# Optimization experiments

Hardware: AMD Instinct MI355X
Metric: run time of the kernel (lower is better)

Reference implementation:

```python
import jax, jax.numpy as jnp
import numpy as np

T, B, Y = 256, 2048, 20   # time, batch, y_dim
H = 256                   # rnn_macro_dim
HD = 256                  # h_dim (decoder MLP)
N_LAYERS = 2


def _gru_cell(x, h, Wih, Whh, bih, bhh):
    # PyTorch GRU cell. Wih: [3H, in], Whh: [3H, H]; gate order r, z, n.
    gx = x @ Wih.T + bih            # [B, 3H]
    gh = h @ Whh.T + bhh            # [B, 3H]
    gx_r, gx_z, gx_n = jnp.split(gx, 3, axis=-1)
    gh_r, gh_z, gh_n = jnp.split(gh, 3, axis=-1)
    r = jax.nn.sigmoid(gx_r + gh_r)
    z = jax.nn.sigmoid(gx_z + gh_z)
    n = jnp.tanh(gx_n + r * gh_n)
    return (1.0 - z) * n + z * h


def setup_inputs() -> dict:
    key = jax.random.key(0)
    ks = jax.random.split(key, 16)
    s = 0.05
    inp = {
        'data': jax.random.normal(ks[0], (T, B, Y), dtype=jnp.float32),
        # GRU layer 0 (input Y) and layer 1 (input H)
        'Wih0': jax.random.normal(ks[1], (3 * H, Y), dtype=jnp.float32) * s,
        'Whh0': jax.random.normal(ks[2], (3 * H, H), dtype=jnp.float32) * s,
        'bih0': jax.random.normal(ks[3], (3 * H,), dtype=jnp.float32) * s,
        'bhh0': jax.random.normal(ks[4], (3 * H,), dtype=jnp.float32) * s,
        'Wih1': jax.random.normal(ks[5], (3 * H, H), dtype=jnp.float32) * s,
        'Whh1': jax.random.normal(ks[6], (3 * H, H), dtype=jnp.float32) * s,
        'bih1': jax.random.normal(ks[7], (3 * H,), dtype=jnp.float32) * s,
        'bhh1': jax.random.normal(ks[8], (3 * H,), dtype=jnp.float32) * s,
        # dec_macro: Linear(H, HD) -> ReLU -> Linear(HD, HD) -> ReLU -> Linear(HD, Y)
        'W1': jax.random.normal(ks[9], (HD, H), dtype=jnp.float32) * s,
        'b1': jax.random.normal(ks[10], (HD,), dtype=jnp.float32) * s,
        'W2': jax.random.normal(ks[11], (HD, HD), dtype=jnp.float32) * s,
        'b2': jax.random.normal(ks[12], (HD,), dtype=jnp.float32) * s,
        'W3': jax.random.normal(ks[13], (Y, HD), dtype=jnp.float32) * s,
        'b3': jax.random.normal(ks[14], (Y,), dtype=jnp.float32) * s,
    }
    return inp


def reference(data, Wih0, Whh0, bih0, bhh0, Wih1, Whh1, bih1, bhh1,
              W1, b1, W2, b2, W3, b3):
    # hp['train'] == 'macro' branch of PROG_RNN_DET.forward
    batch = data.shape[1]
    h_init = jnp.zeros((N_LAYERS, batch, H), dtype=data.dtype)

    def step(h, xs):
        x_t, next_t = xs
        h0 = _gru_cell(x_t, h[0], Wih0, Whh0, bih0, bhh0)
        h1 = _gru_cell(h0, h[1], Wih1, Whh1, bih1, bhh1)
        d = jax.nn.relu(h1 @ W1.T + b1)
        d = jax.nn.relu(d @ W2.T + b2)
        d = d @ W3.T + b3
        loss_t = jnp.sum((d - next_t) ** 2)
        return jnp.stack([h0, h1]), loss_t

    _, losses = jax.lax.scan(step, h_init, (data[:-1], data[1:]))
    return jnp.sum(losses)
```

## Files before the change

### kernel.cpp

```cpp
#include <hip/hip_runtime.h>
#include <stdint.h>

typedef __attribute__((ext_vector_type(4))) float f32x4;
typedef __attribute__((ext_vector_type(2))) long lx2;
typedef unsigned short u16;
typedef unsigned char u8;

#define MFMA8(a,b,c) __builtin_amdgcn_mfma_f32_16x16x32_fp8_fp8((a),(b),(c),0,0,0)

static constexpr int T_STEPS = 256;
static constexpr int BATCH   = 2048;
static constexpr int YDIM    = 20;
static constexpr int BS      = 16;
static constexpr int NWG     = BATCH / BS;

static constexpr int NPAIR   = 768;
static constexpr int WS_U16  = NPAIR * 512;

__device__ __forceinline__ float sigm(float x) { return 1.0f / (1.0f + __expf(-x)); }
__device__ __forceinline__ float tanh_fast(float x) {
    float s = __expf(-2.0f * fabsf(x));
    float r = (1.0f - s) / (1.0f + s);
    return copysignf(r, x);
}
__device__ __forceinline__ f32x4 zero4() { f32x4 v = {0.f,0.f,0.f,0.f}; return v; }
__device__ __forceinline__ u8 f2f8(float v) {
    return (u8)(__builtin_amdgcn_cvt_pk_fp8_f32(v, v, 0, false) & 0xff);
}

__device__ float sval(int P, int half, int l16, int k8,
                      const float* __restrict__ Wih0, const float* __restrict__ Whh0,
                      const float* __restrict__ Wih1, const float* __restrict__ Whh1,
                      const float* __restrict__ W1,   const float* __restrict__ W2,
                      const float* __restrict__ W3) {
    if (P < 192) { int kb=P/24, r=P%24, g=r>>3, wv=r&7, c=wv+8*half;
        return Whh0[(g*256 + c*16 + l16)*256 + kb*32 + k8]; }
    if (P < 224) { int r=P-192; if (r>=24) return 0.f;
        int g=r>>3, wv=r&7, c=wv+8*half, row=g*256+c*16+l16;
        return (k8 < YDIM) ? Wih0[row*YDIM + k8] : 0.f; }
    if (P < 416) { int r=P-224, kb=r/24, rr=r%24, g=rr>>3, wv=rr&7, c=wv+8*half;
        return Whh1[(g*256 + c*16 + l16)*256 + kb*32 + k8]; }
    if (P < 608) { int r=P-416, kb=r/24, rr=r%24, g=rr>>3, wv=rr&7, c=wv+8*half;
        return Wih1[(g*256 + c*16 + l16)*256 + kb*32 + k8]; }
    if (P < 672) { int r=P-608, kb=r>>3, wv=r&7, row=(wv+8*half)*16+l16;
        return W1[row*256 + kb*32 + k8]; }
    if (P < 736) { int r=P-672, kb=r>>3, wv=r&7, row=(wv+8*half)*16+l16;
        return W2[row*256 + kb*32 + k8]; }
    { int r=P-736, s=r>>3, wv=r&7;
      if (wv < 2) { int kb = 2*s + half, row = wv*16 + l16;
          return (row < YDIM) ? W3[row*256 + kb*32 + k8] : 0.f; }
      return 0.f; }
}

__global__ void prep_kernel(const float* __restrict__ Wih0, const float* __restrict__ Whh0,
                            const float* __restrict__ Wih1, const float* __restrict__ Whh1,
                            const float* __restrict__ W1,   const float* __restrict__ W2,
                            const float* __restrict__ W3,   u16* __restrict__ ws,
                            float* __restrict__ out) {
    int tid = blockIdx.x * blockDim.x + threadIdx.x;
    if (tid == 0) out[0] = 0.0f;
    int stride = gridDim.x * blockDim.x;
    for (int m = tid; m < WS_U16; m += stride) {
        int byte0 = 2 * m;
        int P = byte0 >> 10, rem = byte0 & 1023;
        int L = rem >> 4, half = (rem >> 3) & 1, j0 = rem & 7;
        int l16 = L & 15, kqb = (L >> 4) * 8;
        float v0 = sval(P, half, l16, kqb + j0,     Wih0, Whh0, Wih1, Whh1, W1, W2, W3);
        float v1 = sval(P, half, l16, kqb + j0 + 1, Wih0, Whh0, Wih1, Whh1, W1, W2, W3);
        ws[m] = (u16)(__builtin_amdgcn_cvt_pk_fp8_f32(v0, v1, 0, false) & 0xffff);
    }
}

#define BARX() do {                                                 \
    asm volatile("s_waitcnt lgkmcnt(0)" ::: "memory");              \
    __builtin_amdgcn_sched_barrier(0);                              \
    __builtin_amdgcn_s_barrier();                                   \
    __builtin_amdgcn_sched_barrier(0);                              \
} while (0)

#define GM2(ACC, A, PV) do { ACC[0] = MFMA8((A), (PV).x, ACC[0]);   \
                             ACC[1] = MFMA8((A), (PV).y, ACC[1]); } while (0)
#define AFB(S, KT) (*(const long*)&(S)[l16][(KT) * 32 + kq8])
#define LOADC(R0, R1, R2, R3, C) do {                               \
    const u8* b_ = wsl + (size_t)(C) * 32768 + woff;                \
    R0 = *(const lx2*)(b_);          R1 = *(const lx2*)(b_ + 8192); \
    R2 = *(const lx2*)(b_ + 16384); R3 = *(const lx2*)(b_ + 24576); \
} while (0)
#define XCH_A(P0,P1,P2,P3, S, KB, AR,AZ,AN) do {                    \
    const long a0_ = AFB(S, KB), a1_ = AFB(S, (KB)+1);              \
    GM2(AR,a0_,P0); GM2(AZ,a0_,P1); GM2(AN,a0_,P2); GM2(AR,a1_,P3); } while (0)
#define XCH_B(P0,P1,P2,P3, S, KB, AR,AZ,AN) do {                    \
    const long a0_ = AFB(S, KB), a1_ = AFB(S, (KB)+1);              \
    GM2(AZ,a0_,P0); GM2(AN,a0_,P1); GM2(AR,a1_,P2); GM2(AZ,a1_,P3); } while (0)
#define XCH_C(P0,P1,P2,P3, S, KB, AR,AZ,AN) do {                    \
    const long a0_ = AFB(S, KB), a1_ = AFB(S, (KB)+1);              \
    GM2(AN,a0_,P0); GM2(AR,a1_,P1); GM2(AZ,a1_,P2); GM2(AN,a1_,P3); } while (0)
#define XCH_M(P0,P1,P2,P3, S, KB0) do {                             \
    const long m0_ = AFB(S, KB0),     m1_ = AFB(S, (KB0)+1);        \
    const long m2_ = AFB(S, (KB0)+2), m3_ = AFB(S, (KB0)+3);        \
    d0 = MFMA8(m0_, P0.x, d0);  d1v = MFMA8(m0_, P0.y, d1v);        \
    d0 = MFMA8(m1_, P1.x, d0);  d1v = MFMA8(m1_, P1.y, d1v);        \
    d0 = MFMA8(m2_, P2.x, d0);  d1v = MFMA8(m2_, P2.y, d1v);        \
    d0 = MFMA8(m3_, P3.x, d0);  d1v = MFMA8(m3_, P3.y, d1v);        \
} while (0)
#define COMBINE(HSH, HR, BRv, BZv, BXNv, BHNv, AR, AZ, AXN, AHN) do {            \
    _Pragma("unroll") for (int jj = 0; jj < 2; ++jj) {                           \
        const int colb_ = (w + 8 * jj) * 16 + l16;                               \
        _Pragma("unroll") for (int q = 0; q < 4; ++q) {                          \
            const float r_ = sigm(AR[jj][q] + BRv[jj]);                          \
            const float z_ = sigm(AZ[jj][q] + BZv[jj]);                          \
            const float n_ = tanh_fast(AXN[jj][q] + BXNv[jj] + r_ * (AHN[jj][q] + BHNv[jj])); \
            const float hn_ = (1.0f - z_) * n_ + z_ * HR[jj][q];                 \
            HR[jj][q] = hn_;                                                     \
            HSH[kq * 4 + q][colb_] = f2f8(hn_); } }                              \
} while (0)
#define DWRITE(DSH, SB) do {                                                     \
    _Pragma("unroll") for (int q = 0; q < 4; ++q) {                              \
        DSH[kq * 4 + q][w * 16 + l16]       = f2f8(fmaxf(d0[q]  + SB[0], 0.f));  \
        DSH[kq * 4 + q][(8 + w) * 16 + l16] = f2f8(fmaxf(d1v[q] + SB[1], 0.f)); }\
} while (0)
#define ZACC(A) do { A[0] = zero4(); A[1] = zero4(); } while (0)

__global__ __launch_bounds__(512, 1) void rnn_main(
    const float* __restrict__ data,
    const float* __restrict__ bih0g, const float* __restrict__ bhh0g,
    const float* __restrict__ bih1g, const float* __restrict__ bhh1g,
    const float* __restrict__ b1g,  const float* __restrict__ b2g,
    const float* __restrict__ b3g,
    const u16* __restrict__ ws, float* __restrict__ out)
{
    __shared__ __align__(16) u8 sh_h0[2][16][272];
    __shared__ __align__(16) u8 sh_h1[2][16][272];
    __shared__ __align__(16) u8 sh_d1[16][272];
    __shared__ __align__(16) u8 sh_d2[16][272];
    __shared__ __align__(16) u8 sh_x[16][32];

    const int tid  = threadIdx.x;
    const int w    = tid >> 6;
    const int lane = tid & 63;
    const int l16  = lane & 15;
    const int kq   = lane >> 4;
    const int kq8  = kq * 8;
    const int b0   = blockIdx.x * BS;
    const int xr   = tid / YDIM, xc = tid - xr * YDIM;
    const size_t woff = (size_t)w * 1024 + (size_t)lane * 16;

    for (int i = tid; i < 2 * 16 * 272; i += 512) { (&sh_h0[0][0][0])[i] = 0; (&sh_h1[0][0][0])[i] = 0; }
    for (int i = tid; i < 16 * 32;  i += 512) (&sh_x[0][0])[i] = 0;
    if (tid < BS * YDIM) sh_x[xr][xc] = f2f8(data[(size_t)b0 * YDIM + tid]);

    float bR0[2], bZ0[2], bXN0[2], bHN0[2], bR1[2], bZ1[2], bXN1[2], bHN1[2], s1r[2], s2r[2];
    #pragma unroll
    for (int jj = 0; jj < 2; ++jj) {
        const int colb = (w + 8 * jj) * 16 + l16;
        bR0[jj]  = bih0g[colb] + bhh0g[colb];
        bZ0[jj]  = bih0g[colb + 256] + bhh0g[colb + 256];
        bXN0[jj] = bih0g[colb + 512];  bHN0[jj] = bhh0g[colb + 512];
        bR1[jj]  = bih1g[colb] + bhh1g[colb];
        bZ1[jj]  = bih1g[colb + 256] + bhh1g[colb + 256];
        bXN1[jj] = bih1g[colb + 512];  bHN1[jj] = bhh1g[colb + 512];
        s1r[jj]  = b1g[colb];  s2r[jj] = b2g[colb];
    }
    float s3r = 0.0f;
    { const int col = w * 16 + l16; if (w < 2 && col < YDIM) s3r = b3g[col]; }

    float hr0[2][4] = {{0,0,0,0},{0,0,0,0}};
    float hr1[2][4] = {{0,0,0,0},{0,0,0,0}};
    f32x4 r0[2], z0[2], xn0[2], hn0[2];
    f32x4 r1[2], z1[2], xn1[2], hn1[2];
    f32x4 d0, d1v;
    lx2 p00, p01, p02, p03, p10, p11, p12, p13, p20, p21, p22, p23;

    __syncthreads();

    {
        const u8* wsl = (const u8*)ws;
        LOADC(p00, p01, p02, p03, 0);
        LOADC(p10, p11, p12, p13, 1);
        LOADC(p20, p21, p22, p23, 2);
    }
    float loss = 0.0f;

    #pragma unroll 1
    for (int t = 0; t < T_STEPS - 1; ++t) {
        const u8* wsl = (const u8*)ws;
        asm volatile("" : "+s"(wsl));
        u8 (*h0o)[272] = sh_h0[t & 1];  u8 (*h0n)[272] = sh_h0[(t & 1) ^ 1];
        u8 (*h1o)[272] = sh_h1[t & 1];  u8 (*h1n)[272] = sh_h1[(t & 1) ^ 1];

        ZACC(r0); ZACC(z0); ZACC(xn0); ZACC(hn0);
        ZACC(r1); ZACC(z1); ZACC(xn1); ZACC(hn1);

        XCH_A(p00,p01,p02,p03, h0o, 0, r0,z0,hn0);  LOADC(p00,p01,p02,p03, 3);
        XCH_B(p10,p11,p12,p13, h0o, 1, r0,z0,hn0);  LOADC(p10,p11,p12,p13, 4);
        XCH_C(p20,p21,p22,p23, h0o, 2, r0,z0,hn0);  LOADC(p20,p21,p22,p23, 5);
        XCH_A(p00,p01,p02,p03, h0o, 4, r0,z0,hn0);  LOADC(p00,p01,p02,p03, 6);
        XCH_B(p10,p11,p12,p13, h0o, 5, r0,z0,hn0);  LOADC(p10,p11,p12,p13, 7);
        XCH_C(p20,p21,p22,p23, h0o, 6, r0,z0,hn0);  LOADC(p20,p21,p22,p23, 8);
        {
            const long ax = *(const long*)&sh_x[l16][kq8];
            GM2(r0, ax, p00); GM2(z0, ax, p01); GM2(xn0, ax, p02);
        }
        LOADC(p00,p01,p02,p03, 9);
        XCH_A(p10,p11,p12,p13, h1o, 0, r1,z1,hn1);  LOADC(p10,p11,p12,p13, 10);
        XCH_B(p20,p21,p22,p23, h1o, 1, r1,z1,hn1);  LOADC(p20,p21,p22,p23, 11);
        XCH_C(p00,p01,p02,p03, h1o, 2, r1,z1,hn1);  LOADC(p00,p01,p02,p03, 12);
        XCH_A(p10,p11,p12,p13, h1o, 4, r1,z1,hn1);  LOADC(p10,p11,p12,p13, 13);
        XCH_B(p20,p21,p22,p23, h1o, 5, r1,z1,hn1);  LOADC(p20,p21,p22,p23, 14);
        XCH_C(p00,p01,p02,p03, h1o, 6, r1,z1,hn1);  LOADC(p00,p01,p02,p03, 15);
        COMBINE(h0n, hr0, bR0, bZ0, bXN0, bHN0, r0, z0, xn0, hn0);
        BARX();
        XCH_A(p10,p11,p12,p13, h0n, 0, r1,z1,xn1);  LOADC(p10,p11,p12,p13, 16);
        XCH_B(p20,p21,p22,p23, h0n, 1, r1,z1,xn1);  LOADC(p20,p21,p22,p23, 17);
        XCH_C(p00,p01,p02,p03, h0n, 2, r1,z1,xn1);  LOADC(p00,p01,p02,p03, 18);
        XCH_A(p10,p11,p12,p13, h0n, 4, r1,z1,xn1);  LOADC(p10,p11,p12,p13, 19);
        XCH_B(p20,p21,p22,p23, h0n, 5, r1,z1,xn1);  LOADC(p20,p21,p22,p23, 20);
        XCH_C(p00,p01,p02,p03, h0n, 6, r1,z1,xn1);  LOADC(p00,p01,p02,p03, 21);
        COMBINE(h1n, hr1, bR1, bZ1, bXN1, bHN1, r1, z1, xn1, hn1);
        BARX();
        d0 = zero4(); d1v = zero4();
        float xv = 0.f, tg0 = 0.f, tg1 = 0.f, tg2 = 0.f, tg3 = 0.f;
        {
            const float* tp = data + (size_t)(t + 1) * (BATCH * YDIM) + (size_t)b0 * YDIM;
            if (tid < BS * YDIM) xv = tp[tid];
            if (w < 2) {
                const int col = w * 16 + l16;
                if (col < YDIM) {
                    tg0 = tp[(kq * 4 + 0) * YDIM + col];
                    tg1 = tp[(kq * 4 + 1) * YDIM + col];
                    tg2 = tp[(kq * 4 + 2) * YDIM + col];
                    tg3 = tp[(kq * 4 + 3) * YDIM + col];
                }
            }
        }
        XCH_M(p10,p11,p12,p13, h1n, 0);  LOADC(p10,p11,p12,p13, 22);
        XCH_M(p20,p21,p22,p23, h1n, 4);  LOADC(p20,p21,p22,p23, 23);
        DWRITE(sh_d1, s1r);
        BARX();
        d0 = zero4(); d1v = zero4();
        XCH_M(p00,p01,p02,p03, sh_d1, 0);  LOADC(p00,p01,p02,p03, 0);
        XCH_M(p10,p11,p12,p13, sh_d1, 4);  LOADC(p10,p11,p12,p13, 1);
        DWRITE(sh_d2, s2r);
        BARX();
        if (w < 2) {
            f32x4 lacc = zero4();
            lacc = MFMA8(AFB(sh_d2, 0), p20.x, lacc);
            lacc = MFMA8(AFB(sh_d2, 1), p20.y, lacc);
            lacc = MFMA8(AFB(sh_d2, 2), p21.x, lacc);
            lacc = MFMA8(AFB(sh_d2, 3), p21.y, lacc);
            lacc = MFMA8(AFB(sh_d2, 4), p22.x, lacc);
            lacc = MFMA8(AFB(sh_d2, 5), p22.y, lacc);
            lacc = MFMA8(AFB(sh_d2, 6), p23.x, lacc);
            lacc = MFMA8(AFB(sh_d2, 7), p23.y, lacc);
            const int col = w * 16 + l16;
            if (col < YDIM) {
                const float e0 = lacc[0] + s3r - tg0;
                const float e1 = lacc[1] + s3r - tg1;
                const float e2 = lacc[2] + s3r - tg2;
                const float e3 = lacc[3] + s3r - tg3;
                loss += e0 * e0 + e1 * e1 + e2 * e2 + e3 * e3;
            }
        }
        LOADC(p20,p21,p22,p23, 2);
        if (tid < BS * YDIM) sh_x[xr][xc] = f2f8(xv);
        BARX();
    }

    #pragma unroll
    for (int s = 32; s > 0; s >>= 1) loss += __shfl_down(loss, s, 64);
    if (lane == 0 && w < 2) atomicAdd(out, loss);
}

extern "C" void kernel_launch(void* const* d_in, const int* in_sizes, int n_in,
                              void* d_out, int out_size, void* d_ws, size_t ws_size,
                              hipStream_t stream) {
    const float* data = (const float*)d_in[0];
    const float* Wih0 = (const float*)d_in[1];
    const float* Whh0 = (const float*)d_in[2];
    const float* bih0 = (const float*)d_in[3];
    const float* bhh0 = (const float*)d_in[4];
    const float* Wih1 = (const float*)d_in[5];
    const float* Whh1 = (const float*)d_in[6];
    const float* bih1 = (const float*)d_in[7];
    const float* bhh1 = (const float*)d_in[8];
    const float* W1   = (const float*)d_in[9];
    const float* b1   = (const float*)d_in[10];
    const float* W2   = (const float*)d_in[11];
    const float* b2   = (const float*)d_in[12];
    const float* W3   = (const float*)d_in[13];
    const float* b3   = (const float*)d_in[14];
    u16*   ws  = (u16*)d_ws;
    float* out = (float*)d_out;

    hipLaunchKernelGGL(prep_kernel, dim3(512), dim3(256), 0, stream,
                       Wih0, Whh0, Wih1, Whh1, W1, W2, W3, ws, out);
    hipLaunchKernelGGL(rnn_main, dim3(NWG), dim3(512), 0, stream,
                       data, bih0, bhh0, bih1, bhh1, b1, b2, b3, ws, out);
}
```

Measured before the change: 2.201 ms.

## Stage Whh0/Wih0 fp8 weights in LDS and pin decoder weights in registers

```diff
diff --git a/kernel.cpp b/kernel.cpp
--- a/kernel.cpp
+++ b/kernel.cpp
@@ -27,6 +27,7 @@
 __device__ __forceinline__ u8 f2f8(float v) {
     return (u8)(__builtin_amdgcn_cvt_pk_fp8_f32(v, v, 0, false) & 0xff);
 }
+__device__ __forceinline__ void pinv(lx2& v) { asm volatile("" : "+v"(v)); }
 
 __device__ float sval(int P, int half, int l16, int k8,
                       const float* __restrict__ Wih0, const float* __restrict__ Whh0,
@@ -86,6 +87,7 @@
     R0 = *(const lx2*)(b_);          R1 = *(const lx2*)(b_ + 8192); \
     R2 = *(const lx2*)(b_ + 16384); R3 = *(const lx2*)(b_ + 24576); \
 } while (0)
+#define LP(BASE, P) (*(const lx2*)&(BASE)[(size_t)(P) * 1024 + (size_t)lane * 16])
 #define XCH_A(P0,P1,P2,P3, S, KB, AR,AZ,AN) do {                    \
     const long a0_ = AFB(S, KB), a1_ = AFB(S, (KB)+1);              \
     GM2(AR,a0_,P0); GM2(AZ,a0_,P1); GM2(AN,a0_,P2); GM2(AR,a1_,P3); } while (0)
@@ -129,6 +131,8 @@
     const float* __restrict__ b3g,
     const u16* __restrict__ ws, float* __restrict__ out)
 {
+    __shared__ __align__(16) u8 lds_whh0[3 * 32768];
+    __shared__ __align__(16) u8 lds_wih0[32768];
     __shared__ __align__(16) u8 sh_h0[2][16][272];
     __shared__ __align__(16) u8 sh_h1[2][16][272];
     __shared__ __align__(16) u8 sh_d1[16][272];
@@ -144,6 +148,28 @@
     const int b0   = blockIdx.x * BS;
     const int xr   = tid / YDIM, xc = tid - xr * YDIM;
     const size_t woff = (size_t)w * 1024 + (size_t)lane * 16;
+
+    {
+        const lx2* s = (const lx2*)ws;
+        lx2* dW = (lx2*)lds_whh0;
+        lx2* dX = (lx2*)lds_wih0;
+        for (int i = tid; i < 6144; i += 512) dW[i] = s[i];
+        for (int i = tid; i < 2048; i += 512) dX[i] = s[12288 + i];
+    }
+    lx2 w1r[8], w2r[8], w3r[4];
+    {
+        const u8* b = (const u8*)ws;
+        #pragma unroll
+        for (int s = 0; s < 4; ++s) {
+            w1r[s]     = *(const lx2*)(b + (size_t)((19*32 + s*8 + w)) * 1024 + (size_t)lane * 16);
+            w1r[4 + s] = *(const lx2*)(b + (size_t)((20*32 + s*8 + w)) * 1024 + (size_t)lane * 16);
+            w2r[s]     = *(const lx2*)(b + (size_t)((21*32 + s*8 + w)) * 1024 + (size_t)lane * 16);
+            w2r[4 + s] = *(const lx2*)(b + (size_t)((22*32 + s*8 + w)) * 1024 + (size_t)lane * 16);
+            w3r[s]     = *(const lx2*)(b + (size_t)((23*32 + s*8 + w)) * 1024 + (size_t)lane * 16);
+        }
+        #pragma unroll
+        for (int s = 0; s < 4; ++s) { pinv(w1r[s]); pinv(w1r[4+s]); pinv(w2r[s]); pinv(w2r[4+s]); pinv(w3r[s]); }
+    }
 
     for (int i = tid; i < 2 * 16 * 272; i += 512) { (&sh_h0[0][0][0])[i] = 0; (&sh_h1[0][0][0])[i] = 0; }
     for (int i = tid; i < 16 * 32;  i += 512) (&sh_x[0][0])[i] = 0;
@@ -175,9 +201,9 @@
 
     {
         const u8* wsl = (const u8*)ws;
-        LOADC(p00, p01, p02, p03, 0);
-        LOADC(p10, p11, p12, p13, 1);
-        LOADC(p20, p21, p22, p23, 2);
+        LOADC(p00, p01, p02, p03, 3);
+        LOADC(p10, p11, p12, p13, 4);
+        LOADC(p20, p21, p22, p23, 5);
     }
     float loss = 0.0f;
 
@@ -191,31 +217,34 @@
         ZACC(r0); ZACC(z0); ZACC(xn0); ZACC(hn0);
         ZACC(r1); ZACC(z1); ZACC(xn1); ZACC(hn1);
 
-        XCH_A(p00,p01,p02,p03, h0o, 0, r0,z0,hn0);  LOADC(p00,p01,p02,p03, 3);
-        XCH_B(p10,p11,p12,p13, h0o, 1, r0,z0,hn0);  LOADC(p10,p11,p12,p13, 4);
-        XCH_C(p20,p21,p22,p23, h0o, 2, r0,z0,hn0);  LOADC(p20,p21,p22,p23, 5);
-        XCH_A(p00,p01,p02,p03, h0o, 4, r0,z0,hn0);  LOADC(p00,p01,p02,p03, 6);
-        XCH_B(p10,p11,p12,p13, h0o, 5, r0,z0,hn0);  LOADC(p10,p11,p12,p13, 7);
-        XCH_C(p20,p21,p22,p23, h0o, 6, r0,z0,hn0);  LOADC(p20,p21,p22,p23, 8);
+        {   lx2 q0=LP(lds_whh0, w),      q1=LP(lds_whh0, 8+w),  q2=LP(lds_whh0, 16+w), q3=LP(lds_whh0, 24+w);
+            XCH_A(q0,q1,q2,q3, h0o, 0, r0,z0,hn0); }
+        {   lx2 q0=LP(lds_whh0, 32+w),   q1=LP(lds_whh0, 40+w), q2=LP(lds_whh0, 48+w), q3=LP(lds_whh0, 56+w);
+            XCH_B(q0,q1,q2,q3, h0o, 1, r0,z0,hn0); }
+        {   lx2 q0=LP(lds_whh0, 64+w),   q1=LP(lds_whh0, 72+w), q2=LP(lds_whh0, 80+w), q3=LP(lds_whh0, 88+w);
+            XCH_C(q0,q1,q2,q3, h0o, 2, r0,z0,hn0); }
+        XCH_A(p00,p01,p02,p03, h0o, 4, r0,z0,hn0);  LOADC(p00,p01,p02,p03, 7);
+        XCH_B(p10,p11,p12,p13, h0o, 5, r0,z0,hn0);  LOADC(p10,p11,p12,p13, 8);
+        XCH_C(p20,p21,p22,p23, h0o, 6, r0,z0,hn0);  LOADC(p20,p21,p22,p23, 9);
         {
             const long ax = *(const long*)&sh_x[l16][kq8];
-            GM2(r0, ax, p00); GM2(z0, ax, p01); GM2(xn0, ax, p02);
+            lx2 q0=LP(lds_wih0, w), q1=LP(lds_wih0, 8+w), q2=LP(lds_wih0, 16+w);
+            GM2(r0, ax, q0); GM2(z0, ax, q1); GM2(xn0, ax, q2);
         }
-        LOADC(p00,p01,p02,p03, 9);
-        XCH_A(p10,p11,p12,p13, h1o, 0, r1,z1,hn1);  LOADC(p10,p11,p12,p13, 10);
-        XCH_B(p20,p21,p22,p23, h1o, 1, r1,z1,hn1);  LOADC(p20,p21,p22,p23, 11);
-        XCH_C(p00,p01,p02,p03, h1o, 2, r1,z1,hn1);  LOADC(p00,p01,p02,p03, 12);
-        XCH_A(p10,p11,p12,p13, h1o, 4, r1,z1,hn1);  LOADC(p10,p11,p12,p13, 13);
-        XCH_B(p20,p21,p22,p23, h1o, 5, r1,z1,hn1);  LOADC(p20,p21,p22,p23, 14);
-        XCH_C(p00,p01,p02,p03, h1o, 6, r1,z1,hn1);  LOADC(p00,p01,p02,p03, 15);
+        XCH_A(p00,p01,p02,p03, h1o, 0, r1,z1,hn1);  LOADC(p00,p01,p02,p03, 10);
+        XCH_B(p10,p11,p12,p13, h1o, 1, r1,z1,hn1);  LOADC(p10,p11,p12,p13, 11);
+        XCH_C(p20,p21,p22,p23, h1o, 2, r1,z1,hn1);  LOADC(p20,p21,p22,p23, 12);
+        XCH_A(p00,p01,p02,p03, h1o, 4, r1,z1,hn1);  LOADC(p00,p01,p02,p03, 13);
+        XCH_B(p10,p11,p12,p13, h1o, 5, r1,z1,hn1);  LOADC(p10,p11,p12,p13, 14);
+        XCH_C(p20,p21,p22,p23, h1o, 6, r1,z1,hn1);  LOADC(p20,p21,p22,p23, 15);
         COMBINE(h0n, hr0, bR0, bZ0, bXN0, bHN0, r0, z0, xn0, hn0);
         BARX();
-        XCH_A(p10,p11,p12,p13, h0n, 0, r1,z1,xn1);  LOADC(p10,p11,p12,p13, 16);
-        XCH_B(p20,p21,p22,p23, h0n, 1, r1,z1,xn1);  LOADC(p20,p21,p22,p23, 17);
-        XCH_C(p00,p01,p02,p03, h0n, 2, r1,z1,xn1);  LOADC(p00,p01,p02,p03, 18);
-        XCH_A(p10,p11,p12,p13, h0n, 4, r1,z1,xn1);  LOADC(p10,p11,p12,p13, 19);
-        XCH_B(p20,p21,p22,p23, h0n, 5, r1,z1,xn1);  LOADC(p20,p21,p22,p23, 20);
-        XCH_C(p00,p01,p02,p03, h0n, 6, r1,z1,xn1);  LOADC(p00,p01,p02,p03, 21);
+        XCH_A(p00,p01,p02,p03, h0n, 0, r1,z1,xn1);  LOADC(p00,p01,p02,p03, 16);
+        XCH_B(p10,p11,p12,p13, h0n, 1, r1,z1,xn1);  LOADC(p10,p11,p12,p13, 17);
+        XCH_C(p20,p21,p22,p23, h0n, 2, r1,z1,xn1);  LOADC(p20,p21,p22,p23, 18);
+        XCH_A(p00,p01,p02,p03, h0n, 4, r1,z1,xn1);  LOADC(p00,p01,p02,p03, 3);
+        XCH_B(p10,p11,p12,p13, h0n, 5, r1,z1,xn1);  LOADC(p10,p11,p12,p13, 4);
+        XCH_C(p20,p21,p22,p23, h0n, 6, r1,z1,xn1);  LOADC(p20,p21,p22,p23, 5);
         COMBINE(h1n, hr1, bR1, bZ1, bXN1, bHN1, r1, z1, xn1, hn1);
         BARX();
         d0 = zero4(); d1v = zero4();
@@ -233,25 +262,25 @@
                 }
             }
         }
-        XCH_M(p10,p11,p12,p13, h1n, 0);  LOADC(p10,p11,p12,p13, 22);
-        XCH_M(p20,p21,p22,p23, h1n, 4);  LOADC(p20,p21,p22,p23, 23);
+        XCH_M(w1r[0], w1r[1], w1r[2], w1r[3], h1n, 0);
+        XCH_M(w1r[4], w1r[5], w1r[6], w1r[7], h1n, 4);
         DWRITE(sh_d1, s1r);
         BARX();
         d0 = zero4(); d1v = zero4();
-        XCH_M(p00,p01,p02,p03, sh_d1, 0);  LOADC(p00,p01,p02,p03, 0);
-        XCH_M(p10,p11,p12,p13, sh_d1, 4);  LOADC(p10,p11,p12,p13, 1);
+        XCH_M(w2r[0], w2r[1], w2r[2], w2r[3], sh_d1, 0);
+        XCH_M(w2r[4], w2r[5], w2r[6], w2r[7], sh_d1, 4);
         DWRITE(sh_d2, s2r);
         BARX();
         if (w < 2) {
             f32x4 lacc = zero4();
-            lacc = MFMA8(AFB(sh_d2, 0), p20.x, lacc);
-            lacc = MFMA8(AFB(sh_d2, 1), p20.y, lacc);
-            lacc = MFMA8(AFB(sh_d2, 2), p21.x, lacc);
-            lacc = MFMA8(AFB(sh_d2, 3), p21.y, lacc);
-            lacc = MFMA8(AFB(sh_d2, 4), p22.x, lacc);
-            lacc = MFMA8(AFB(sh_d2, 5), p22.y, lacc);
-            lacc = MFMA8(AFB(sh_d2, 6), p23.x, lacc);
-            lacc = MFMA8(AFB(sh_d2, 7), p23.y, lacc);
+            lacc = MFMA8(AFB(sh_d2, 0), w3r[0].x, lacc);
+            lacc = MFMA8(AFB(sh_d2, 1), w3r[0].y, lacc);
+            lacc = MFMA8(AFB(sh_d2, 2), w3r[1].x, lacc);
+            lacc = MFMA8(AFB(sh_d2, 3), w3r[1].y, lacc);
+            lacc = MFMA8(AFB(sh_d2, 4), w3r[2].x, lacc);
+            lacc = MFMA8(AFB(sh_d2, 5), w3r[2].y, lacc);
+            lacc = MFMA8(AFB(sh_d2, 6), w3r[3].x, lacc);
+            lacc = MFMA8(AFB(sh_d2, 7), w3r[3].y, lacc);
             const int col = w * 16 + l16;
             if (col < YDIM) {
                 const float e0 = lacc[0] + s3r - tg0;
@@ -261,11 +290,11 @@
                 loss += e0 * e0 + e1 * e1 + e2 * e2 + e3 * e3;
             }
         }
-        LOADC(p20,p21,p22,p23, 2);
         if (tid < BS * YDIM) sh_x[xr][xc] = f2f8(xv);
         BARX();
     }
 
+    asm volatile("s_waitcnt vmcnt(0)" ::: "memory");
     #pragma unroll
     for (int s = 32; s > 0; s >>= 1) loss += __shfl_down(loss, s, 64);
     if (lane == 0 && w < 2) atomicAdd(out, loss);
```

Result: slower. 2.814 ms (+27.8%).
